# Kernel tuning notes

Measured on AMD Instinct MI355X. Metric: run time of the kernel, lower is better.

## Reference

```python
import jax, jax.numpy as jnp
import numpy as np

B_J0 = 0.01   # baseline threshold
DT = 1.0
BETA = 1.8    # adaptation strength
LENS = 0.5
SCALE = 6.0
HIGHT = 0.15
GAMMA = 0.5


def _gauss(x, mu, sigma):
    return jnp.exp(-(x - mu) ** 2 / (2.0 * sigma ** 2)) / jnp.sqrt(2.0 * jnp.pi) / sigma


@jax.custom_vjp
def spike_fn(x):
    return (x > 0).astype(x.dtype)


def _spike_fwd(x):
    return spike_fn(x), x


def _spike_bwd(x, g):
    # multi-gaussian surrogate gradient (config.gradient_type == 'MG')
    temp = (_gauss(x, 0.0, LENS) * (1.0 + HIGHT)
            - _gauss(x, LENS, SCALE * LENS) * HIGHT
            - _gauss(x, -LENS, SCALE * LENS) * HIGHT)
    return (g * temp * GAMMA,)


spike_fn.defvjp(_spike_fwd, _spike_bwd)


def setup_inputs() -> dict:
    key = jax.random.key(0)
    ks = jax.random.split(key, 20)
    Bt, T, I, H, O = 256, 250, 700, 128, 20
    f32 = jnp.float32
    return {
        'x': jax.random.uniform(ks[0], (Bt, T, I), dtype=f32),
        'mask': jnp.ones((2, H, H), dtype=f32),
        'w_ih1': (jax.random.normal(ks[1], (I, H), dtype=f32) / np.sqrt(I).astype(np.float32)),
        'b_ih1': jnp.zeros((H,), f32),
        'w_h1h1': (jax.random.normal(ks[2], (H, H), dtype=f32) / np.sqrt(H).astype(np.float32)),
        'b_h1h1': jnp.zeros((H,), f32),
        'w_h1h2': (jax.random.normal(ks[3], (H, H), dtype=f32) / np.sqrt(H).astype(np.float32)),
        'b_h1h2': jnp.zeros((H,), f32),
        'w_h2h2': (jax.random.normal(ks[4], (H, H), dtype=f32) / np.sqrt(H).astype(np.float32)),
        'b_h2h2': jnp.zeros((H,), f32),
        'w_h2o': (jax.random.normal(ks[5], (H, O), dtype=f32) / np.sqrt(H).astype(np.float32)),
        'b_h2o': jnp.zeros((O,), f32),
        'tau_adp_h1': 150.0 + 10.0 * jax.random.normal(ks[6], (H,), dtype=f32),
        'tau_adp_h2': 150.0 + 10.0 * jax.random.normal(ks[7], (H,), dtype=f32),
        'tau_m_h1': 20.0 + 5.0 * jax.random.normal(ks[8], (H,), dtype=f32),
        'tau_m_h2': 20.0 + 5.0 * jax.random.normal(ks[9], (H,), dtype=f32),
        'tau_m_o': 20.0 + 5.0 * jax.random.normal(ks[10], (O,), dtype=f32),
        'hid1_mem0': jax.random.uniform(ks[11], (Bt, H), dtype=f32),
        'hid2_mem0': jax.random.uniform(ks[12], (Bt, H), dtype=f32),
        'out_mem0': jax.random.uniform(ks[13], (Bt, O), dtype=f32),
    }


def _forward(x, mask, w_ih1, b_ih1, w_h1h1, b_h1h1, w_h1h2, b_h1h2,
             w_h2h2, b_h2h2, w_h2o, b_h2o, tau_adp_h1, tau_adp_h2,
             tau_m_h1, tau_m_h2, tau_m_o, hid1_mem0, hid2_mem0, out_mem0):
    Bt, T, _ = x.shape
    H = w_ih1.shape[1]
    O = w_h2o.shape[1]
    # dropout mask applied to recurrent weights (weights stored [in, out])
    w11 = w_h1h1 * mask[0]
    w22 = w_h2h2 * mask[1]
    a1 = jnp.exp(-DT / tau_m_h1)
    r1 = jnp.exp(-DT / tau_adp_h1)
    a2 = jnp.exp(-DT / tau_m_h2)
    r2 = jnp.exp(-DT / tau_adp_h2)
    ao = jnp.exp(-DT / tau_m_o)
    # precompute input projection for all timesteps: [T, B, H]
    xin = jnp.einsum('bti,ih->tbh', x, w_ih1) + b_ih1

    def step(carry, inps):
        h1m, h1s, h2m, h2s, om, b1, b2, acc, s1, s2 = carry
        xt, t = inps
        # layer 1 (adaptive LIF)
        i1 = xt + h1s @ w11 + b_h1h1
        b1 = r1 * b1 + (1.0 - r1) * h1s
        B1 = B_J0 + BETA * b1
        h1m = h1m * a1 + (1.0 - a1) * i1 - B1 * h1s * DT
        h1s = spike_fn(h1m - B1)
        s1 = s1 + h1s
        # layer 2 (adaptive LIF)
        i2 = h1s @ w_h1h2 + b_h1h2 + h2s @ w22 + b_h2h2
        b2 = r2 * b2 + (1.0 - r2) * h2s
        B2 = B_J0 + BETA * b2
        h2m = h2m * a2 + (1.0 - a2) * i2 - B2 * h2s * DT
        h2s = spike_fn(h2m - B2)
        s2 = s2 + h2s
        # leaky-integrator readout (no spike)
        io = h2s @ w_h2o + b_h2o
        om = om * ao + (1.0 - ao) * io
        acc = acc + jnp.where(t > 10, jax.nn.softmax(om, axis=-1), 0.0)
        return (h1m, h1s, h2m, h2s, om, b1, b2, acc, s1, s2), None

    zH = jnp.zeros((Bt, H), x.dtype)
    carry0 = (hid1_mem0, zH, hid2_mem0, zH, out_mem0,
              jnp.full((Bt, H), B_J0, x.dtype), jnp.full((Bt, H), B_J0, x.dtype),
              jnp.zeros((Bt, O), x.dtype), zH, zH)
    carry, _ = jax.lax.scan(step, carry0, (xin, jnp.arange(T)))
    output, s1, s2 = carry[7], carry[8], carry[9]
    A_norm = jnp.sum(jnp.abs(w11)) + jnp.sum(jnp.abs(w22))
    return output, s1 / T, s2 / T, A_norm


def reference(x, mask, w_ih1, b_ih1, w_h1h1, b_h1h1, w_h1h2, b_h1h2,
              w_h2h2, b_h2h2, w_h2o, b_h2o, tau_adp_h1, tau_adp_h2,
              tau_m_h1, tau_m_h2, tau_m_o, hid1_mem0, hid2_mem0, out_mem0):
    return _forward(x, mask, w_ih1, b_ih1, w_h1h1, b_h1h1, w_h1h2, b_h1h2,
                    w_h2h2, b_h2h2, w_h2o, b_h2o, tau_adp_h1, tau_adp_h2,
                    tau_m_h1, tau_m_h2, tau_m_o, hid1_mem0, hid2_mem0, out_mem0)
```

## Files before the change

kernel.cpp:

```cpp
#include <hip/hip_runtime.h>
#include <math.h>

#define TT 250
#define BT 256
#define HN 128
#define ON 20
#define KIN 700
#define NKT 22

#define XIN_OFF 0
#define WPKH_OFF 8192000
#define WPKL_OFF 8237056

typedef __attribute__((ext_vector_type(8))) short bf16x8;
typedef __attribute__((ext_vector_type(4))) float f32x4;

__device__ __forceinline__ unsigned short bf16rne(float f) {
    unsigned u = __float_as_uint(f);
    unsigned r = u + 0x7fffu + ((u >> 16) & 1u);
    return (unsigned short)(r >> 16);
}
__device__ __forceinline__ void hilo(float v, short& h, short& l) {
    unsigned short hh = bf16rne(v);
    float vh = __uint_as_float((unsigned)hh << 16);
    h = (short)hh;
    l = (short)bf16rne(v - vh);
}

__device__ __forceinline__ void gl_lds16(const void* g, void* l) {
    __builtin_amdgcn_global_load_lds(
        (const __attribute__((address_space(1))) unsigned int*)g,
        (__attribute__((address_space(3))) unsigned int*)l, 16, 0, 0);
}

__global__ __launch_bounds__(256) void packw(const float* __restrict__ w,
                                             unsigned short* __restrict__ ph,
                                             unsigned short* __restrict__ pl) {
    int i = blockIdx.x * 256 + threadIdx.x;
    int k = i >> 7, c = i & 127;
    float v = (k < KIN) ? w[k * HN + c] : 0.f;
    short h, l;
    hilo(v, h, l);
    int dst = (((k >> 5) * 8 + (c >> 4)) * 64 + (((k >> 3) & 3) * 16 + (c & 15))) * 8 + (k & 7);
    ph[dst] = (unsigned short)h;
    pl[dst] = (unsigned short)l;
}

__device__ __forceinline__ void stage_kt(const unsigned short* __restrict__ wph,
                                         const unsigned short* __restrict__ wpl,
                                         void* buf, int kt, int tid) {
    const char* sh = (const char*)wph + kt * 8192 + tid * 16;
    const char* sl = (const char*)wpl + kt * 8192 + tid * 16;
    char* b = (char*)buf;
    const int wb = (tid >> 6) * 1024;
    gl_lds16(sh,        b + wb);
    gl_lds16(sh + 4096, b + wb + 4096);
    gl_lds16(sl,        b + wb + 8192);
    gl_lds16(sl + 4096, b + wb + 12288);
}

__device__ __forceinline__ void loadx8(float* av, const float* p, bool tailq3) {
    *(float4*)&av[0] = *(const float4*)p;
    if (tailq3) {
        av[4] = 0.f; av[5] = 0.f; av[6] = 0.f; av[7] = 0.f;
    } else {
        *(float4*)&av[4] = *(const float4*)(p + 4);
    }
}

__global__ __launch_bounds__(256, 2) void gemm_in(const float* __restrict__ x,
        const unsigned short* __restrict__ wph, const unsigned short* __restrict__ wpl,
        const float* __restrict__ bias1, const float* __restrict__ bias2,
        float* __restrict__ xin) {
    __shared__ __align__(16) unsigned char wbuf[2][16384];
    const int tid = threadIdx.x;
    const int w = tid >> 6, lane = tid & 63;
    const int q = lane >> 4, li = lane & 15;
    const long mbase = (long)blockIdx.x * 128;
    const float* xr0 = x + (mbase + w * 16 + li) * KIN + q * 8;

    f32x4 acc[2][8];
#pragma unroll
    for (int c = 0; c < 2; c++)
#pragma unroll
        for (int nt = 0; nt < 8; nt++) acc[c][nt] = (f32x4){0.f, 0.f, 0.f, 0.f};

    stage_kt(wph, wpl, wbuf[0], 0, tid);
    float av[2][8];
    loadx8(av[0], xr0, false);
    loadx8(av[1], xr0 + 64 * KIN, false);
    __syncthreads();

    for (int kt = 0; kt < NKT; kt++) {
        if (kt + 1 < NKT)
            stage_kt(wph, wpl, wbuf[(kt + 1) & 1], kt + 1, tid);
        const bf16x8* cv = (const bf16x8*)&wbuf[kt & 1][0];
#pragma unroll
        for (int c = 0; c < 2; c++) {
            bf16x8 ah, al;
#pragma unroll
            for (int j = 0; j < 8; j++) {
                short h, l;
                hilo(av[c][j], h, l);
                ah[j] = h; al[j] = l;
            }
            if (kt + 1 < NKT)
                loadx8(av[c], xr0 + c * (64 * KIN) + (kt + 1) * 32,
                       (kt + 1 == NKT - 1) && (q == 3));
#pragma unroll
            for (int nt = 0; nt < 8; nt++) {
                bf16x8 bh = cv[nt * 64 + lane];
                bf16x8 bl = cv[512 + nt * 64 + lane];
                acc[c][nt] = __builtin_amdgcn_mfma_f32_16x16x32_bf16(ah, bh, acc[c][nt], 0, 0, 0);
                acc[c][nt] = __builtin_amdgcn_mfma_f32_16x16x32_bf16(al, bh, acc[c][nt], 0, 0, 0);
                acc[c][nt] = __builtin_amdgcn_mfma_f32_16x16x32_bf16(ah, bl, acc[c][nt], 0, 0, 0);
            }
        }
        __syncthreads();
    }

    float b12[8];
#pragma unroll
    for (int nt = 0; nt < 8; nt++) {
        int c = nt * 16 + li;
        b12[nt] = bias1[c] + bias2[c];
    }
#pragma unroll
    for (int c = 0; c < 2; c++) {
#pragma unroll
        for (int r = 0; r < 4; r++) {
            long m = mbase + c * 64 + w * 16 + q * 4 + r;
            int bq = (int)(((unsigned long long)m * 67109ull) >> 24);
            int tt = (int)m - bq * 250;
            float* dst = xin + ((size_t)tt * BT + bq) * HN;
#pragma unroll
            for (int nt = 0; nt < 8; nt++) dst[nt * 16 + li] = acc[c][nt][r] + b12[nt];
        }
    }
}

__global__ __launch_bounds__(512, 2) void snn_scan(
    const float* __restrict__ xin, const float* __restrict__ mask,
    const float* __restrict__ w_h1h1, const float* __restrict__ w_h1h2,
    const float* __restrict__ b_h1h2, const float* __restrict__ w_h2h2,
    const float* __restrict__ b_h2h2, const float* __restrict__ w_h2o,
    const float* __restrict__ b_h2o, const float* __restrict__ tau_adp1,
    const float* __restrict__ tau_adp2, const float* __restrict__ taum1,
    const float* __restrict__ taum2, const float* __restrict__ taumo,
    const float* __restrict__ h1m0, const float* __restrict__ h2m0,
    const float* __restrict__ om0, float* __restrict__ out) {

    __shared__ __align__(16) unsigned short sA1[2048];
    __shared__ __align__(16) unsigned short sA2[2048];
    __shared__ float omb[16 * ON];
    __shared__ float red[8];

    const int tid = threadIdx.x;
    const int w = tid >> 6, lane = tid & 63;
    const int q = lane >> 4, li = lane & 15;
    const int col = w * 16 + li;
    const int r0 = blockIdx.x * 16;

    bf16x8 h11[4], l11[4], h22[4], l22[4], h12[4], l12[4], hO[4], lO[4];
    const int ocol = (w == 6) ? li : 16 + li;
    const bool oval = (w >= 6) && (ocol < ON);
    float pn = 0.f;
#pragma unroll
    for (int kt = 0; kt < 4; kt++) {
#pragma unroll
        for (int j = 0; j < 8; j++) {
            const int k = kt * 32 + q * 8 + j;
            const int idx = k * HN + col;
            float v11 = w_h1h1[idx] * mask[idx];
            float v22 = w_h2h2[idx] * mask[HN * HN + idx];
            float v12 = w_h1h2[idx];
            pn += fabsf(v11) + fabsf(v22);
            short hh, ll;
            hilo(v11, hh, ll); h11[kt][j] = hh; l11[kt][j] = ll;
            hilo(v22, hh, ll); h22[kt][j] = hh; l22[kt][j] = ll;
            hilo(v12, hh, ll); h12[kt][j] = hh; l12[kt][j] = ll;
            float vO = oval ? w_h2o[k * ON + ocol] : 0.f;
            hilo(vO, hh, ll); hO[kt][j] = hh; lO[kt][j] = ll;
        }
    }

    const float a1 = expf(-1.f / taum1[col]);
    const float r1 = expf(-1.f / tau_adp1[col]);
    const float a2 = expf(-1.f / taum2[col]);
    const float r2 = expf(-1.f / tau_adp2[col]);
    const float cc2 = b_h1h2[col] + b_h2h2[col];
    float h1m[4], h2m[4], b1[4], b2[4], c1[4], c2n[4];
    unsigned s1bits = 0, s2bits = 0;
#pragma unroll
    for (int r = 0; r < 4; r++) {
        h1m[r] = h1m0[(r0 + q * 4 + r) * HN + col];
        h2m[r] = h2m0[(r0 + q * 4 + r) * HN + col];
        b1[r] = 0.01f; b2[r] = 0.01f; c1[r] = 0.f; c2n[r] = 0.f;
    }
    const float ao = oval ? expf(-1.f / taumo[ocol]) : 0.f;
    const float bo = oval ? b_h2o[ocol] : 0.f;
    float om[4];
#pragma unroll
    for (int r = 0; r < 4; r++)
        om[r] = oval ? om0[(r0 + q * 4 + r) * ON + ocol] : 0.f;
    const int sm = lane >> 2, ob = (lane & 3) * 5;
    float accs[5] = {0.f, 0.f, 0.f, 0.f, 0.f};

    {
        unsigned* z1 = (unsigned*)sA1;
        unsigned* z2 = (unsigned*)sA2;
        z1[tid & 511] = 0u; z1[(tid & 511) + 512] = 0u;
        z2[tid & 511] = 0u; z2[(tid & 511) + 512] = 0u;
    }

#pragma unroll
    for (int off = 32; off > 0; off >>= 1) pn += __shfl_down(pn, off);
    if (lane == 0) red[w] = pn;
    __syncthreads();
    if (tid == 0 && blockIdx.x == 0) {
        float s = 0.f;
#pragma unroll
        for (int i = 0; i < 8; i++) s += red[i];
        out[70656] = s;
    }

    const int wbase = (w >> 1) * 512 + (((2 * w + (li >> 3)) & 3) * 16 + q * 4) * 8 + (li & 7);

    const bf16x8* sa1v = (const bf16x8*)sA1;
    const bf16x8* sa2v = (const bf16x8*)sA2;
    const unsigned short ONE = 0x3F80u;

    bf16x8 g1[4];
    const bf16x8 zf = {0, 0, 0, 0, 0, 0, 0, 0};
#pragma unroll
    for (int kt = 0; kt < 4; kt++) g1[kt] = zf;

    const float* xp = xin + (size_t)(r0 + q * 4) * HN + col;

    for (int t = 0; t < TT; t++) {
        float xt[4];
#pragma unroll
        for (int r = 0; r < 4; r++) xt[r] = xp[r * HN];
        xp += BT * HN;

        bf16x8 f2[4];
#pragma unroll
        for (int kt = 0; kt < 4; kt++) f2[kt] = sa2v[kt * 64 + lane];
        f32x4 aI = {0.f, 0.f, 0.f, 0.f}, aG = {0.f, 0.f, 0.f, 0.f};
#pragma unroll
        for (int kt = 0; kt < 4; kt++) {
            aI = __builtin_amdgcn_mfma_f32_16x16x32_bf16(g1[kt], h11[kt], aI, 0, 0, 0);
            aI = __builtin_amdgcn_mfma_f32_16x16x32_bf16(g1[kt], l11[kt], aI, 0, 0, 0);
            aG = __builtin_amdgcn_mfma_f32_16x16x32_bf16(f2[kt], h22[kt], aG, 0, 0, 0);
            aG = __builtin_amdgcn_mfma_f32_16x16x32_bf16(f2[kt], l22[kt], aG, 0, 0, 0);
        }
        if (w >= 6) {
            f32x4 aO = {0.f, 0.f, 0.f, 0.f};
#pragma unroll
            for (int kt = 0; kt < 4; kt++) {
                aO = __builtin_amdgcn_mfma_f32_16x16x32_bf16(f2[kt], hO[kt], aO, 0, 0, 0);
                aO = __builtin_amdgcn_mfma_f32_16x16x32_bf16(f2[kt], lO[kt], aO, 0, 0, 0);
            }
            if (t >= 1) {
#pragma unroll
                for (int r = 0; r < 4; r++) {
                    om[r] = ao * om[r] + (1.f - ao) * (bo + aO[r]);
                    if (oval) omb[(q * 4 + r) * ON + ocol] = om[r];
                }
            }
        }
#pragma unroll
        for (int r = 0; r < 4; r++) {
            const float sv = (float)((s1bits >> r) & 1u);
            const float i1 = xt[r] + aI[r];
            b1[r] = r1 * b1[r] + (1.f - r1) * sv;
            const float B = 0.01f + 1.8f * b1[r];
            h1m[r] = a1 * h1m[r] + (1.f - a1) * i1 - B * sv;
            const bool sp = (h1m[r] - B) > 0.f;
            s1bits = sp ? (s1bits | (1u << r)) : (s1bits & ~(1u << r));
            c1[r] += sp ? 1.f : 0.f;
            sA1[wbase + r * 8] = sp ? ONE : (unsigned short)0;
        }
        __syncthreads();

#pragma unroll
        for (int kt = 0; kt < 4; kt++) g1[kt] = sa1v[kt * 64 + lane];
        f32x4 aJ = {0.f, 0.f, 0.f, 0.f};
#pragma unroll
        for (int kt = 0; kt < 4; kt++) {
            aJ = __builtin_amdgcn_mfma_f32_16x16x32_bf16(g1[kt], h12[kt], aJ, 0, 0, 0);
            aJ = __builtin_amdgcn_mfma_f32_16x16x32_bf16(g1[kt], l12[kt], aJ, 0, 0, 0);
        }
        if (w == 0 && t >= 12) {
            float v[5], e[5];
            float mx = -1e30f;
#pragma unroll
            for (int i = 0; i < 5; i++) { v[i] = omb[sm * ON + ob + i]; mx = fmaxf(mx, v[i]); }
            mx = fmaxf(mx, __shfl_xor(mx, 1));
            mx = fmaxf(mx, __shfl_xor(mx, 2));
            float se = 0.f;
#pragma unroll
            for (int i = 0; i < 5; i++) { e[i] = __expf(v[i] - mx); se += e[i]; }
            se += __shfl_xor(se, 1);
            se += __shfl_xor(se, 2);
            const float inv = 1.f / se;
#pragma unroll
            for (int i = 0; i < 5; i++) accs[i] += e[i] * inv;
        }
#pragma unroll
        for (int r = 0; r < 4; r++) {
            const float sv = (float)((s2bits >> r) & 1u);
            const float i2 = aJ[r] + aG[r] + cc2;
            b2[r] = r2 * b2[r] + (1.f - r2) * sv;
            const float B = 0.01f + 1.8f * b2[r];
            h2m[r] = a2 * h2m[r] + (1.f - a2) * i2 - B * sv;
            const bool sp = (h2m[r] - B) > 0.f;
            s2bits = sp ? (s2bits | (1u << r)) : (s2bits & ~(1u << r));
            c2n[r] += sp ? 1.f : 0.f;
            sA2[wbase + r * 8] = sp ? ONE : (unsigned short)0;
        }
        __syncthreads();
    }

    if (w >= 6) {
        bf16x8 f2[4];
#pragma unroll
        for (int kt = 0; kt < 4; kt++) f2[kt] = sa2v[kt * 64 + lane];
        f32x4 aO = {0.f, 0.f, 0.f, 0.f};
#pragma unroll
        for (int kt = 0; kt < 4; kt++) {
            aO = __builtin_amdgcn_mfma_f32_16x16x32_bf16(f2[kt], hO[kt], aO, 0, 0, 0);
            aO = __builtin_amdgcn_mfma_f32_16x16x32_bf16(f2[kt], lO[kt], aO, 0, 0, 0);
        }
#pragma unroll
        for (int r = 0; r < 4; r++) {
            om[r] = ao * om[r] + (1.f - ao) * (bo + aO[r]);
            if (oval) omb[(q * 4 + r) * ON + ocol] = om[r];
        }
    }
    __syncthreads();
    if (w == 0) {
        float v[5], e[5];
        float mx = -1e30f;
#pragma unroll
        for (int i = 0; i < 5; i++) { v[i] = omb[sm * ON + ob + i]; mx = fmaxf(mx, v[i]); }
        mx = fmaxf(mx, __shfl_xor(mx, 1));
        mx = fmaxf(mx, __shfl_xor(mx, 2));
        float se = 0.f;
#pragma unroll
        for (int i = 0; i < 5; i++) { e[i] = __expf(v[i] - mx); se += e[i]; }
        se += __shfl_xor(se, 1);
        se += __shfl_xor(se, 2);
        const float inv = 1.f / se;
#pragma unroll
        for (int i = 0; i < 5; i++) out[(r0 + sm) * ON + ob + i] = accs[i] + e[i] * inv;
    }
#pragma unroll
    for (int r = 0; r < 4; r++) {
        out[5120 + (r0 + q * 4 + r) * HN + col] = c1[r] * (1.f / 250.f);
        out[37888 + (r0 + q * 4 + r) * HN + col] = c2n[r] * (1.f / 250.f);
    }
}

extern "C" void kernel_launch(void* const* d_in, const int* in_sizes, int n_in,
                              void* d_out, int out_size, void* d_ws, size_t ws_size,
                              hipStream_t stream) {
    const float* x        = (const float*)d_in[0];
    const float* mask     = (const float*)d_in[1];
    const float* w_ih1    = (const float*)d_in[2];
    const float* b_ih1    = (const float*)d_in[3];
    const float* w_h1h1   = (const float*)d_in[4];
    const float* b_h1h1   = (const float*)d_in[5];
    const float* w_h1h2   = (const float*)d_in[6];
    const float* b_h1h2   = (const float*)d_in[7];
    const float* w_h2h2   = (const float*)d_in[8];
    const float* b_h2h2   = (const float*)d_in[9];
    const float* w_h2o    = (const float*)d_in[10];
    const float* b_h2o    = (const float*)d_in[11];
    const float* tau_adp1 = (const float*)d_in[12];
    const float* tau_adp2 = (const float*)d_in[13];
    const float* taum1    = (const float*)d_in[14];
    const float* taum2    = (const float*)d_in[15];
    const float* taumo    = (const float*)d_in[16];
    const float* h1m0     = (const float*)d_in[17];
    const float* h2m0     = (const float*)d_in[18];
    const float* om0      = (const float*)d_in[19];
    float* out = (float*)d_out;
    float* ws  = (float*)d_ws;

    float* xin = ws + XIN_OFF;
    unsigned short* wph = (unsigned short*)(ws + WPKH_OFF);
    unsigned short* wpl = (unsigned short*)(ws + WPKL_OFF);

    packw<<<352, 256, 0, stream>>>(w_ih1, wph, wpl);
    gemm_in<<<500, 256, 0, stream>>>(x, wph, wpl, b_ih1, b_h1h1, xin);
    snn_scan<<<16, 512, 0, stream>>>(xin, mask, w_h1h1, w_h1h2, b_h1h2, w_h2h2,
                                     b_h2h2, w_h2o, b_h2o, tau_adp1, tau_adp2,
                                     taum1, taum2, taumo, h1m0, h2m0, om0, out);
}
```

Baseline: 609.7 us.

## Skew layer-2 and readout by one step to halve per-timestep barriers

Restructures the recurrent scan as a software pipeline. Layer 2 and the readout run one timestep behind layer 1, and the spike buffers and readout buffer are double-buffered in shared memory. Each iteration now needs a single __syncthreads instead of two, and all MFMAs for a step can issue together. The cost is double the LDS for the spike and output buffers, plus extra epilogue code to drain the pipeline, which adds complexity and a risk of off-by-one errors in the timestep indexing.

```diff
diff --git a/kernel.cpp b/kernel.cpp
--- a/kernel.cpp
+++ b/kernel.cpp
@@ -150,9 +150,9 @@
     const float* __restrict__ h1m0, const float* __restrict__ h2m0,
     const float* __restrict__ om0, float* __restrict__ out) {
 
-    __shared__ __align__(16) unsigned short sA1[2048];
-    __shared__ __align__(16) unsigned short sA2[2048];
-    __shared__ float omb[16 * ON];
+    __shared__ __align__(16) unsigned short sA1[2 * 2048];
+    __shared__ __align__(16) unsigned short sA2[2 * 2048];
+    __shared__ float omb[2][16 * ON];
     __shared__ float red[8];
 
     const int tid = threadIdx.x;
@@ -209,8 +209,8 @@
     {
         unsigned* z1 = (unsigned*)sA1;
         unsigned* z2 = (unsigned*)sA2;
-        z1[tid & 511] = 0u; z1[(tid & 511) + 512] = 0u;
-        z2[tid & 511] = 0u; z2[(tid & 511) + 512] = 0u;
+        z1[tid] = 0u; z1[tid + 512] = 0u; z1[tid + 1024] = 0u; z1[tid + 1536] = 0u;
+        z2[tid] = 0u; z2[tid + 512] = 0u; z2[tid + 1024] = 0u; z2[tid + 1536] = 0u;
     }
 
 #pragma unroll
@@ -225,135 +225,221 @@
     }
 
     const int wbase = (w >> 1) * 512 + (((2 * w + (li >> 3)) & 3) * 16 + q * 4) * 8 + (li & 7);
-
-    const bf16x8* sa1v = (const bf16x8*)sA1;
-    const bf16x8* sa2v = (const bf16x8*)sA2;
     const unsigned short ONE = 0x3F80u;
 
-    bf16x8 g1[4];
-    const bf16x8 zf = {0, 0, 0, 0, 0, 0, 0, 0};
-#pragma unroll
-    for (int kt = 0; kt < 4; kt++) g1[kt] = zf;
-
     const float* xp = xin + (size_t)(r0 + q * 4) * HN + col;
 
-    for (int t = 0; t < TT; t++) {
+    for (int i = 0; i < TT; i++) {
+        const int pa = i & 1;
+
         float xt[4];
 #pragma unroll
         for (int r = 0; r < 4; r++) xt[r] = xp[r * HN];
         xp += BT * HN;
 
-        bf16x8 f2[4];
-#pragma unroll
-        for (int kt = 0; kt < 4; kt++) f2[kt] = sa2v[kt * 64 + lane];
-        f32x4 aI = {0.f, 0.f, 0.f, 0.f}, aG = {0.f, 0.f, 0.f, 0.f};
+        const bf16x8* g1p = (const bf16x8*)(sA1 + ((pa ^ 1) << 11));
+        const bf16x8* f2p = (const bf16x8*)(sA2 + (pa << 11));
+        bf16x8 g1[4], f2[4];
+#pragma unroll
+        for (int kt = 0; kt < 4; kt++) {
+            g1[kt] = g1p[kt * 64 + lane];
+            f2[kt] = f2p[kt * 64 + lane];
+        }
+
+        f32x4 aI = {0.f, 0.f, 0.f, 0.f}, aJ = {0.f, 0.f, 0.f, 0.f}, aG = {0.f, 0.f, 0.f, 0.f};
 #pragma unroll
         for (int kt = 0; kt < 4; kt++) {
             aI = __builtin_amdgcn_mfma_f32_16x16x32_bf16(g1[kt], h11[kt], aI, 0, 0, 0);
             aI = __builtin_amdgcn_mfma_f32_16x16x32_bf16(g1[kt], l11[kt], aI, 0, 0, 0);
+            aJ = __builtin_amdgcn_mfma_f32_16x16x32_bf16(g1[kt], h12[kt], aJ, 0, 0, 0);
+            aJ = __builtin_amdgcn_mfma_f32_16x16x32_bf16(g1[kt], l12[kt], aJ, 0, 0, 0);
             aG = __builtin_amdgcn_mfma_f32_16x16x32_bf16(f2[kt], h22[kt], aG, 0, 0, 0);
             aG = __builtin_amdgcn_mfma_f32_16x16x32_bf16(f2[kt], l22[kt], aG, 0, 0, 0);
         }
+        f32x4 aO = {0.f, 0.f, 0.f, 0.f};
         if (w >= 6) {
-            f32x4 aO = {0.f, 0.f, 0.f, 0.f};
 #pragma unroll
             for (int kt = 0; kt < 4; kt++) {
                 aO = __builtin_amdgcn_mfma_f32_16x16x32_bf16(f2[kt], hO[kt], aO, 0, 0, 0);
                 aO = __builtin_amdgcn_mfma_f32_16x16x32_bf16(f2[kt], lO[kt], aO, 0, 0, 0);
             }
-            if (t >= 1) {
-#pragma unroll
-                for (int r = 0; r < 4; r++) {
-                    om[r] = ao * om[r] + (1.f - ao) * (bo + aO[r]);
-                    if (oval) omb[(q * 4 + r) * ON + ocol] = om[r];
-                }
-            }
-        }
-#pragma unroll
-        for (int r = 0; r < 4; r++) {
-            const float sv = (float)((s1bits >> r) & 1u);
-            const float i1 = xt[r] + aI[r];
-            b1[r] = r1 * b1[r] + (1.f - r1) * sv;
-            const float B = 0.01f + 1.8f * b1[r];
-            h1m[r] = a1 * h1m[r] + (1.f - a1) * i1 - B * sv;
-            const bool sp = (h1m[r] - B) > 0.f;
-            s1bits = sp ? (s1bits | (1u << r)) : (s1bits & ~(1u << r));
-            c1[r] += sp ? 1.f : 0.f;
-            sA1[wbase + r * 8] = sp ? ONE : (unsigned short)0;
+        }
+
+        if (i >= 1) {
+            unsigned short* s2w = sA2 + ((pa ^ 1) << 11);
+#pragma unroll
+            for (int r = 0; r < 4; r++) {
+                const float sv = (float)((s2bits >> r) & 1u);
+                const float i2 = aJ[r] + aG[r] + cc2;
+                b2[r] = r2 * b2[r] + (1.f - r2) * sv;
+                const float B = 0.01f + 1.8f * b2[r];
+                h2m[r] = a2 * h2m[r] + (1.f - a2) * i2 - B * sv;
+                const bool sp = (h2m[r] - B) > 0.f;
+                s2bits = sp ? (s2bits | (1u << r)) : (s2bits & ~(1u << r));
+                c2n[r] += sp ? 1.f : 0.f;
+                s2w[wbase + r * 8] = sp ? ONE : (unsigned short)0;
+            }
+        }
+
+        if (w >= 6 && i >= 2) {
+#pragma unroll
+            for (int r = 0; r < 4; r++) {
+                om[r] = ao * om[r] + (1.f - ao) * (bo + aO[r]);
+                if (oval) omb[pa][(q * 4 + r) * ON + ocol] = om[r];
+            }
+        }
+
+        if (w == 0 && i >= 14) {
+            float v[5], e[5];
+            float mx = -1e30f;
+#pragma unroll
+            for (int s = 0; s < 5; s++) { v[s] = omb[pa ^ 1][sm * ON + ob + s]; mx = fmaxf(mx, v[s]); }
+            mx = fmaxf(mx, __shfl_xor(mx, 1));
+            mx = fmaxf(mx, __shfl_xor(mx, 2));
+            float se = 0.f;
+#pragma unroll
+            for (int s = 0; s < 5; s++) { e[s] = __expf(v[s] - mx); se += e[s]; }
+            se += __shfl_xor(se, 1);
+            se += __shfl_xor(se, 2);
+            const float inv = 1.f / se;
+#pragma unroll
+            for (int s = 0; s < 5; s++) accs[s] += e[s] * inv;
+        }
+
+        {
+            unsigned short* s1w = sA1 + (pa << 11);
+#pragma unroll
+            for (int r = 0; r < 4; r++) {
+                const float sv = (float)((s1bits >> r) & 1u);
+                const float i1 = xt[r] + aI[r];
+                b1[r] = r1 * b1[r] + (1.f - r1) * sv;
+                const float B = 0.01f + 1.8f * b1[r];
+                h1m[r] = a1 * h1m[r] + (1.f - a1) * i1 - B * sv;
+                const bool sp = (h1m[r] - B) > 0.f;
+                s1bits = sp ? (s1bits | (1u << r)) : (s1bits & ~(1u << r));
+                c1[r] += sp ? 1.f : 0.f;
+                s1w[wbase + r * 8] = sp ? ONE : (unsigned short)0;
+            }
         }
         __syncthreads();
-
-#pragma unroll
-        for (int kt = 0; kt < 4; kt++) g1[kt] = sa1v[kt * 64 + lane];
-        f32x4 aJ = {0.f, 0.f, 0.f, 0.f};
+    }
+
+    {
+        const bf16x8* g1p = (const bf16x8*)(sA1 + 2048);
+        const bf16x8* f2p = (const bf16x8*)(sA2);
+        bf16x8 g1[4], f2[4];
+#pragma unroll
+        for (int kt = 0; kt < 4; kt++) {
+            g1[kt] = g1p[kt * 64 + lane];
+            f2[kt] = f2p[kt * 64 + lane];
+        }
+        f32x4 aJ = {0.f, 0.f, 0.f, 0.f}, aG = {0.f, 0.f, 0.f, 0.f};
 #pragma unroll
         for (int kt = 0; kt < 4; kt++) {
             aJ = __builtin_amdgcn_mfma_f32_16x16x32_bf16(g1[kt], h12[kt], aJ, 0, 0, 0);
             aJ = __builtin_amdgcn_mfma_f32_16x16x32_bf16(g1[kt], l12[kt], aJ, 0, 0, 0);
-        }
-        if (w == 0 && t >= 12) {
+            aG = __builtin_amdgcn_mfma_f32_16x16x32_bf16(f2[kt], h22[kt], aG, 0, 0, 0);
+            aG = __builtin_amdgcn_mfma_f32_16x16x32_bf16(f2[kt], l22[kt], aG, 0, 0, 0);
+        }
+        f32x4 aO = {0.f, 0.f, 0.f, 0.f};
+        if (w >= 6) {
+#pragma unroll
+            for (int kt = 0; kt < 4; kt++) {
+                aO = __builtin_amdgcn_mfma_f32_16x16x32_bf16(f2[kt], hO[kt], aO, 0, 0, 0);
+                aO = __builtin_amdgcn_mfma_f32_16x16x32_bf16(f2[kt], lO[kt], aO, 0, 0, 0);
+            }
+        }
+        {
+            unsigned short* s2w = sA2 + 2048;
+#pragma unroll
+            for (int r = 0; r < 4; r++) {
+                const float sv = (float)((s2bits >> r) & 1u);
+                const float i2 = aJ[r] + aG[r] + cc2;
+                b2[r] = r2 * b2[r] + (1.f - r2) * sv;
+                const float B = 0.01f + 1.8f * b2[r];
+                h2m[r] = a2 * h2m[r] + (1.f - a2) * i2 - B * sv;
+                const bool sp = (h2m[r] - B) > 0.f;
+                s2bits = sp ? (s2bits | (1u << r)) : (s2bits & ~(1u << r));
+                c2n[r] += sp ? 1.f : 0.f;
+                s2w[wbase + r * 8] = sp ? ONE : (unsigned short)0;
+            }
+        }
+        if (w >= 6) {
+#pragma unroll
+            for (int r = 0; r < 4; r++) {
+                om[r] = ao * om[r] + (1.f - ao) * (bo + aO[r]);
+                if (oval) omb[0][(q * 4 + r) * ON + ocol] = om[r];
+            }
+        }
+        if (w == 0) {
             float v[5], e[5];
             float mx = -1e30f;
 #pragma unroll
-            for (int i = 0; i < 5; i++) { v[i] = omb[sm * ON + ob + i]; mx = fmaxf(mx, v[i]); }
+            for (int s = 0; s < 5; s++) { v[s] = omb[1][sm * ON + ob + s]; mx = fmaxf(mx, v[s]); }
             mx = fmaxf(mx, __shfl_xor(mx, 1));
             mx = fmaxf(mx, __shfl_xor(mx, 2));
             float se = 0.f;
 #pragma unroll
-            for (int i = 0; i < 5; i++) { e[i] = __expf(v[i] - mx); se += e[i]; }
+            for (int s = 0; s < 5; s++) { e[s] = __expf(v[s] - mx); se += e[s]; }
             se += __shfl_xor(se, 1);
             se += __shfl_xor(se, 2);
             const float inv = 1.f / se;
 #pragma unroll
-            for (int i = 0; i < 5; i++) accs[i] += e[i] * inv;
-        }
-#pragma unroll
-        for (int r = 0; r < 4; r++) {
-            const float sv = (float)((s2bits >> r) & 1u);
-            const float i2 = aJ[r] + aG[r] + cc2;
-            b2[r] = r2 * b2[r] + (1.f - r2) * sv;
-            const float B = 0.01f + 1.8f * b2[r];
-            h2m[r] = a2 * h2m[r] + (1.f - a2) * i2 - B * sv;
-            const bool sp = (h2m[r] - B) > 0.f;
-            s2bits = sp ? (s2bits | (1u << r)) : (s2bits & ~(1u << r));
-            c2n[r] += sp ? 1.f : 0.f;
-            sA2[wbase + r * 8] = sp ? ONE : (unsigned short)0;
+            for (int s = 0; s < 5; s++) accs[s] += e[s] * inv;
         }
         __syncthreads();
     }
-
-    if (w >= 6) {
-        bf16x8 f2[4];
-#pragma unroll
-        for (int kt = 0; kt < 4; kt++) f2[kt] = sa2v[kt * 64 + lane];
-        f32x4 aO = {0.f, 0.f, 0.f, 0.f};
-#pragma unroll
-        for (int kt = 0; kt < 4; kt++) {
-            aO = __builtin_amdgcn_mfma_f32_16x16x32_bf16(f2[kt], hO[kt], aO, 0, 0, 0);
-            aO = __builtin_amdgcn_mfma_f32_16x16x32_bf16(f2[kt], lO[kt], aO, 0, 0, 0);
-        }
-#pragma unroll
-        for (int r = 0; r < 4; r++) {
-            om[r] = ao * om[r] + (1.f - ao) * (bo + aO[r]);
-            if (oval) omb[(q * 4 + r) * ON + ocol] = om[r];
-        }
-    }
-    __syncthreads();
+    {
+        if (w >= 6) {
+            const bf16x8* f2p = (const bf16x8*)(sA2 + 2048);
+            bf16x8 f2[4];
+#pragma unroll
+            for (int kt = 0; kt < 4; kt++) f2[kt] = f2p[kt * 64 + lane];
+            f32x4 aO = {0.f, 0.f, 0.f, 0.f};
+#pragma unroll
+            for (int kt = 0; kt < 4; kt++) {
+                aO = __builtin_amdgcn_mfma_f32_16x16x32_bf16(f2[kt], hO[kt], aO, 0, 0, 0);
+                aO = __builtin_amdgcn_mfma_f32_16x16x32_bf16(f2[kt], lO[kt], aO, 0, 0, 0);
+            }
+#pragma unroll
+            for (int r = 0; r < 4; r++) {
+                om[r] = ao * om[r] + (1.f - ao) * (bo + aO[r]);
+                if (oval) omb[1][(q * 4 + r) * ON + ocol] = om[r];
+            }
+        }
+        if (w == 0) {
+            float v[5], e[5];
+            float mx = -1e30f;
+#pragma unroll
+            for (int s = 0; s < 5; s++) { v[s] = omb[0][sm * ON + ob + s]; mx = fmaxf(mx, v[s]); }
+            mx = fmaxf(mx, __shfl_xor(mx, 1));
+            mx = fmaxf(mx, __shfl_xor(mx, 2));
+            float se = 0.f;
+#pragma unroll
+            for (int s = 0; s < 5; s++) { e[s] = __expf(v[s] - mx); se += e[s]; }
+            se += __shfl_xor(se, 1);
+            se += __shfl_xor(se, 2);
+            const float inv = 1.f / se;
+#pragma unroll
+            for (int s = 0; s < 5; s++) accs[s] += e[s] * inv;
+        }
+        __syncthreads();
+    }
     if (w == 0) {
         float v[5], e[5];
         float mx = -1e30f;
 #pragma unroll
-        for (int i = 0; i < 5; i++) { v[i] = omb[sm * ON + ob + i]; mx = fmaxf(mx, v[i]); }
+        for (int s = 0; s < 5; s++) { v[s] = omb[1][sm * ON + ob + s]; mx = fmaxf(mx, v[s]); }
         mx = fmaxf(mx, __shfl_xor(mx, 1));
         mx = fmaxf(mx, __shfl_xor(mx, 2));
         float se = 0.f;
 #pragma unroll
-        for (int i = 0; i < 5; i++) { e[i] = __expf(v[i] - mx); se += e[i]; }
+        for (int s = 0; s < 5; s++) { e[s] = __expf(v[s] - mx); se += e[s]; }
         se += __shfl_xor(se, 1);
         se += __shfl_xor(se, 2);
         const float inv = 1.f / se;
 #pragma unroll
-        for (int i = 0; i < 5; i++) out[(r0 + sm) * ON + ob + i] = accs[i] + e[i] * inv;
+        for (int s = 0; s < 5; s++) out[(r0 + sm) * ON + ob + s] = accs[s] + e[s] * inv;
     }
 #pragma unroll
     for (int r = 0; r < 4; r++) {
```

After: 559.1 us. 1.09x faster.
